# Optimization experiments

Hardware: AMD Instinct MI355X
Metric: run time of the kernel (lower is better)

## Reference

```python
import jax, jax.numpy as jnp
import numpy as np

N_ATOMS = 4_000_000   # number of atoms (batched over the per-atom Python loop)
N_PARTS = 1024        # number of molecular parts (size of atom_charge table)
D = 16                # fixed feature width from Linear(16,16)


def setup_inputs() -> dict:
    key = jax.random.key(0)
    ks = jax.random.split(key, 9)
    atom_type_vector = jax.random.normal(ks[0], (N_ATOMS, D), dtype=jnp.float32)
    atom_charge = jax.random.normal(ks[1], (N_PARTS,), dtype=jnp.float32)
    # three Linear(16,16) layers, PyTorch layout: y = x @ W.T + b
    W1 = jax.random.normal(ks[2], (D, D), dtype=jnp.float32) * 0.25
    b1 = jax.random.normal(ks[3], (D,), dtype=jnp.float32) * 0.1
    W2 = jax.random.normal(ks[4], (D, D), dtype=jnp.float32) * 0.25
    b2 = jax.random.normal(ks[5], (D,), dtype=jnp.float32) * 0.1
    W3 = jax.random.normal(ks[6], (D, D), dtype=jnp.float32) * 0.25
    b3 = jax.random.normal(ks[7], (D,), dtype=jnp.float32) * 0.1
    atom_part = jax.random.randint(ks[8], (N_ATOMS,), 0, N_PARTS, dtype=jnp.int64)
    return {"atom_type_vector": atom_type_vector, "atom_charge": atom_charge,
            "W1": W1, "b1": b1, "W2": W2, "b2": b2, "W3": W3, "b3": b3,
            "atom_part": atom_part}


def reference(atom_type_vector, atom_charge, W1, b1, W2, b2, W3, b3, atom_part):
    # Batched version of the per-atom loop:
    # nodes[i] = MLP(atom_type_vector[i]) + atom_part[i] + atom_charge[atom_part[i]]
    h = jax.nn.elu(atom_type_vector @ W1.T + b1)
    h = jax.nn.elu(h @ W2.T + b2)
    h = jax.nn.elu(h @ W3.T + b3)          # [N, 16]
    add = atom_part.astype(h.dtype) + atom_charge[atom_part]  # [N] broadcast scalars
    return h + add[:, None]
```

## Files before the change

kernel.cpp:

```cpp
#include <hip/hip_runtime.h>
#include <math.h>

#define NPARTS 1024
#define BLOCK 256
#define WPB (BLOCK / 64)
#define T 4
#define GRID_BLOCKS 2048

typedef __attribute__((ext_vector_type(4))) _Float16 half4;
typedef __attribute__((ext_vector_type(4))) float floatx4;

__global__ __launch_bounds__(BLOCK, 6) void nodes_mlp_mfma(
    const float* __restrict__ x,
    const float* __restrict__ charge,
    const float* __restrict__ W1, const float* __restrict__ b1,
    const float* __restrict__ W2, const float* __restrict__ b2,
    const float* __restrict__ W3, const float* __restrict__ b3,
    const int*   __restrict__ part,
    float* __restrict__ out,
    int n)
{
    __shared__ float sq[NPARTS];
    for (int i = threadIdx.x; i < NPARTS; i += BLOCK) sq[i] = charge[i];
    __syncthreads();

    const int lane = threadIdx.x & 63;
    const int col  = lane & 15;
    const int g    = lane >> 4;

    half4  aW[3];
    floatx4 cB[3];
    {
        const float* Ws[3] = {W1, W2, W3};
        const float* bs[3] = {b1, b2, b3};
#pragma unroll
        for (int L = 0; L < 3; ++L) {
            const float4 wv = *(const float4*)(Ws[L] + col * 16 + 4 * g);
            half4 a;
            a[0] = (_Float16)wv.x; a[1] = (_Float16)wv.y;
            a[2] = (_Float16)wv.z; a[3] = (_Float16)wv.w;
            aW[L] = a;
            const float4 bv = *(const float4*)(bs[L] + 4 * g);
            floatx4 c;
            c[0] = bv.x; c[1] = bv.y; c[2] = bv.z; c[3] = bv.w;
            cB[L] = c;
        }
    }

    const int ntiles = (n + 15) >> 4;
    const int nwaves = gridDim.x * WPB;
    const int wid    = blockIdx.x * WPB + (threadIdx.x >> 6);

    for (int t0 = wid * T; t0 < ntiles; t0 += nwaves * T) {

        floatx4 xv[T];
        int     pp[T];
        int     rw[T];
#pragma unroll
        for (int u = 0; u < T; ++u) {
            const int tile = t0 + u;
            const int row  = tile * 16 + col;
            const int rowc = (row < n) ? row : (n - 1);
            rw[u] = row;
            xv[u] = *(const floatx4*)(x + rowc * 16 + 4 * g);
            pp[u] = part[rowc];
        }

#pragma unroll
        for (int u = 0; u < T; ++u) {
            half4 bx;
            bx[0] = (_Float16)xv[u][0]; bx[1] = (_Float16)xv[u][1];
            bx[2] = (_Float16)xv[u][2]; bx[3] = (_Float16)xv[u][3];

            floatx4 d = __builtin_amdgcn_mfma_f32_16x16x16f16(aW[0], bx, cB[0], 0, 0, 0);

            half4 h2;
#pragma unroll
            for (int i = 0; i < 4; ++i) {
                float v = d[i];
                v = (v > 0.0f) ? v : (__expf(v) - 1.0f);
                h2[i] = (_Float16)v;
            }
            d = __builtin_amdgcn_mfma_f32_16x16x16f16(aW[1], h2, cB[1], 0, 0, 0);

            half4 h3;
#pragma unroll
            for (int i = 0; i < 4; ++i) {
                float v = d[i];
                v = (v > 0.0f) ? v : (__expf(v) - 1.0f);
                h3[i] = (_Float16)v;
            }
            d = __builtin_amdgcn_mfma_f32_16x16x16f16(aW[2], h3, cB[2], 0, 0, 0);

            const int   p   = pp[u];
            const float add = (float)p + sq[p];

            floatx4 r;
            {
                float v0 = d[0]; v0 = (v0 > 0.0f) ? v0 : (__expf(v0) - 1.0f);
                float v1 = d[1]; v1 = (v1 > 0.0f) ? v1 : (__expf(v1) - 1.0f);
                float v2 = d[2]; v2 = (v2 > 0.0f) ? v2 : (__expf(v2) - 1.0f);
                float v3 = d[3]; v3 = (v3 > 0.0f) ? v3 : (__expf(v3) - 1.0f);
                r[0] = v0 + add; r[1] = v1 + add; r[2] = v2 + add; r[3] = v3 + add;
            }

            if (rw[u] < n) {
                __builtin_nontemporal_store(r, (floatx4*)(out + rw[u] * 16 + 4 * g));
            }
        }
    }
}

extern "C" void kernel_launch(void* const* d_in, const int* in_sizes, int n_in,
                              void* d_out, int out_size, void* d_ws, size_t ws_size,
                              hipStream_t stream) {
    const float* x      = (const float*)d_in[0];
    const float* charge = (const float*)d_in[1];
    const float* W1     = (const float*)d_in[2];
    const float* b1     = (const float*)d_in[3];
    const float* W2     = (const float*)d_in[4];
    const float* b2     = (const float*)d_in[5];
    const float* W3     = (const float*)d_in[6];
    const float* b3     = (const float*)d_in[7];
    const int*   part   = (const int*)d_in[8];
    float* out = (float*)d_out;

    const int n      = in_sizes[8];
    const int ntiles = (n + 15) >> 4;
    int grid = (ntiles + WPB * T - 1) / (WPB * T);
    if (grid > GRID_BLOCKS) grid = GRID_BLOCKS;

    nodes_mlp_mfma<<<grid, BLOCK, 0, stream>>>(
        x, charge, W1, b1, W2, b2, W3, b3, part, out, n);
}
```

Baseline: 455.7 us.

## Double-buffer input loads across grid-stride iterations and raise occupancy bound

Each wave now prefetches the next grid-stride batch of x rows and part indices while it computes the current batch. A sched_barrier keeps the compiler from sinking those prefetch loads into the compute. Tiles per wave per iteration drop from 4 to 2 and the launch bound rises from 6 to 8 blocks per CU, so more waves can hide memory latency. Out-of-range tiles are clamped to the last tile, which is then recomputed and written again with the same values. The extra register buffers may pressure the tighter register budget.

```diff
diff --git a/kernel.cpp b/kernel.cpp
--- a/kernel.cpp
+++ b/kernel.cpp
@@ -4,13 +4,13 @@
 #define NPARTS 1024
 #define BLOCK 256
 #define WPB (BLOCK / 64)
-#define T 4
+#define T 2
 #define GRID_BLOCKS 2048
 
 typedef __attribute__((ext_vector_type(4))) _Float16 half4;
 typedef __attribute__((ext_vector_type(4))) float floatx4;
 
-__global__ __launch_bounds__(BLOCK, 6) void nodes_mlp_mfma(
+__global__ __launch_bounds__(BLOCK, 8) void nodes_mlp_mfma(
     const float* __restrict__ x,
     const float* __restrict__ charge,
     const float* __restrict__ W1, const float* __restrict__ b1,
@@ -50,27 +50,43 @@
     const int ntiles = (n + 15) >> 4;
     const int nwaves = gridDim.x * WPB;
     const int wid    = blockIdx.x * WPB + (threadIdx.x >> 6);
+    const int stride = nwaves * T;
 
-    for (int t0 = wid * T; t0 < ntiles; t0 += nwaves * T) {
+    int t0 = wid * T;
+    if (t0 >= ntiles) return;
 
-        floatx4 xv[T];
-        int     pp[T];
-        int     rw[T];
+    floatx4 xc[T];
+    int     pc[T];
+#pragma unroll
+    for (int u = 0; u < T; ++u) {
+        int tt   = t0 + u; if (tt > ntiles - 1) tt = ntiles - 1;
+        int row  = tt * 16 + col;
+        int rowc = (row < n) ? row : (n - 1);
+        xc[u] = *(const floatx4*)(x + rowc * 16 + 4 * g);
+        pc[u] = part[rowc];
+    }
+
+    for (; t0 < ntiles; t0 += stride) {
+        floatx4 xn[T];
+        int     pn[T];
 #pragma unroll
         for (int u = 0; u < T; ++u) {
-            const int tile = t0 + u;
-            const int row  = tile * 16 + col;
-            const int rowc = (row < n) ? row : (n - 1);
-            rw[u] = row;
-            xv[u] = *(const floatx4*)(x + rowc * 16 + 4 * g);
-            pp[u] = part[rowc];
+            int tt   = t0 + stride + u; if (tt > ntiles - 1) tt = ntiles - 1;
+            int row  = tt * 16 + col;
+            int rowc = (row < n) ? row : (n - 1);
+            xn[u] = *(const floatx4*)(x + rowc * 16 + 4 * g);
+            pn[u] = part[rowc];
         }
+        __builtin_amdgcn_sched_barrier(0);
 
 #pragma unroll
         for (int u = 0; u < T; ++u) {
+            int tt  = t0 + u; if (tt > ntiles - 1) tt = ntiles - 1;
+            int row = tt * 16 + col;
+
             half4 bx;
-            bx[0] = (_Float16)xv[u][0]; bx[1] = (_Float16)xv[u][1];
-            bx[2] = (_Float16)xv[u][2]; bx[3] = (_Float16)xv[u][3];
+            bx[0] = (_Float16)xc[u][0]; bx[1] = (_Float16)xc[u][1];
+            bx[2] = (_Float16)xc[u][2]; bx[3] = (_Float16)xc[u][3];
 
             floatx4 d = __builtin_amdgcn_mfma_f32_16x16x16f16(aW[0], bx, cB[0], 0, 0, 0);
 
@@ -92,7 +108,7 @@
             }
             d = __builtin_amdgcn_mfma_f32_16x16x16f16(aW[2], h3, cB[2], 0, 0, 0);
 
-            const int   p   = pp[u];
+            const int   p   = pc[u];
             const float add = (float)p + sq[p];
 
             floatx4 r;
@@ -104,10 +120,13 @@
                 r[0] = v0 + add; r[1] = v1 + add; r[2] = v2 + add; r[3] = v3 + add;
             }
 
-            if (rw[u] < n) {
-                __builtin_nontemporal_store(r, (floatx4*)(out + rw[u] * 16 + 4 * g));
+            if (row < n) {
+                __builtin_nontemporal_store(r, (floatx4*)(out + row * 16 + 4 * g));
             }
         }
+
+#pragma unroll
+        for (int u = 0; u < T; ++u) { xc[u] = xn[u]; pc[u] = pn[u]; }
     }
 }
 
```

Result: no change. 455.1 us (-0.1%).
